# Performance work log

Hardware: AMD Instinct MI355X
Metric: run time of the kernel (lower is better)

## Reference

```python
import jax, jax.numpy as jnp
import numpy as np

N_NODES = 100000
IN_F = 256
OUT_F = 128
N_EDGES = 1600000


def setup_inputs() -> dict:
    key = jax.random.key(0)
    k1, k2, k3, k4, k5 = jax.random.split(key, 5)
    x = jax.random.normal(k1, (N_NODES, IN_F), dtype=jnp.float32)
    edge_index = jax.random.randint(k2, (2, N_EDGES), 0, N_NODES, dtype=jnp.int64)
    edge_weight = jax.random.uniform(k3, (N_EDGES,), dtype=jnp.float32)
    # Xavier-uniform init as in reset_parameters
    limit = float(np.sqrt(6.0 / (IN_F + OUT_F)))
    weight = jax.random.uniform(k4, (IN_F, OUT_F), dtype=jnp.float32,
                                minval=-limit, maxval=limit)
    return {"x": x, "edge_index": edge_index, "edge_weight": edge_weight,
            "weight": weight}


def reference(x, edge_index, edge_weight, weight):
    # support = X @ W  -- dense feature transform
    support = x @ weight                       # [N, out_f]
    # output = spmm(adj, support): out[dst] += w_e * support[src]
    dst = edge_index[0]
    src = edge_index[1]
    msgs = support[src] * edge_weight[:, None]  # [E, out_f] gather
    out = jax.ops.segment_sum(msgs, dst, num_segments=N_NODES)  # [N, out_f]
    return out
```

## Files before the change

### kernel.cpp

```cpp
#include <hip/hip_runtime.h>

#define N_NODES 100000
#define IN_F 256
#define OUT_F 128
#define NB 782

typedef float f32x4 __attribute__((ext_vector_type(4)));
typedef __bf16 bf16x8 __attribute__((ext_vector_type(8)));

__device__ inline unsigned cvt2_bf16(float a, float b) {
  unsigned ua = __float_as_uint(a), ub = __float_as_uint(b);
  ua = (ua + 0x7fffu + ((ua >> 16) & 1u)) >> 16;
  ub = (ub + 0x7fffu + ((ub >> 16) & 1u)) >> 16;
  return ua | (ub << 16);
}
__device__ inline unsigned short cvt1_bf16(float a) {
  unsigned ua = __float_as_uint(a);
  return (unsigned short)((ua + 0x7fffu + ((ua >> 16) & 1u)) >> 16);
}

__global__ __launch_bounds__(256) void transpose_w(const float* __restrict__ w,
                                                   uint4* __restrict__ wt) {
  int c = blockIdx.x * 256 + threadIdx.x;
  int l = c & 63;
  int kt = (c >> 6) & 7;
  int nt = c >> 9;
  int n = nt * 16 + (l & 15);
  int kb = kt * 32 + ((l >> 4) & 3) * 8;
  unsigned d[4];
#pragma unroll
  for (int j = 0; j < 4; ++j) {
    float a = w[(size_t)(kb + 2 * j) * OUT_F + n];
    float b = w[(size_t)(kb + 2 * j + 1) * OUT_F + n];
    d[j] = cvt2_bf16(a, b);
  }
  wt[c] = make_uint4(d[0], d[1], d[2], d[3]);
}

__global__ __launch_bounds__(256) void gemm_count(const float* __restrict__ x,
                                                  const uint4* __restrict__ wt,
                                                  unsigned short* __restrict__ sup,
                                                  const int* __restrict__ ei,
                                                  int* __restrict__ coarse,
                                                  int nedges, int nblk, int gblocks) {
  __shared__ uint4 As[1024];
  __shared__ uint4 Bs[1024];
  __shared__ int hist[NB];
  const int gid = blockIdx.x;
  const int t = threadIdx.x;

  int role, sub;
  int m = (gblocks < nblk) ? gblocks : nblk;
  if (gid < 2 * m) {
    role = gid & 1;
    sub = gid >> 1;
  } else if (nblk > gblocks) {
    role = 1;
    sub = gid - gblocks;
  } else {
    role = 0;
    sub = gid - nblk;
  }

  if (role == 1) {
    for (int i = t; i < NB; i += 256) hist[i] = 0;
    __syncthreads();
    const int base = sub * 2048;
#pragma unroll
    for (int j = 0; j < 8; ++j) {
      int e = base + j * 256 + t;
      if (e < nedges) atomicAdd(&hist[ei[e] >> 7], 1);
    }
    __syncthreads();
    for (int i = t; i < NB; i += 256) coarse[(size_t)sub * NB + i] = hist[i];
    return;
  }

  const int lane = t & 63;
  const int wv = t >> 6;
  const int wm = wv >> 1, wn = wv & 1;
  const int row0 = sub * 128;

  f32x4 acc[4][4];
#pragma unroll
  for (int mi = 0; mi < 4; ++mi)
#pragma unroll
    for (int ni = 0; ni < 4; ++ni) acc[mi][ni] = (f32x4){0.f, 0.f, 0.f, 0.f};

  for (int it = 0; it < 4; ++it) {
    const int k0 = it * 64;
#pragma unroll
    for (int i = 0; i < 4; ++i) {
      int ci = i * 256 + t;
      int g = ci >> 6, l = ci & 63;
      int mrow = (g >> 1) * 16 + (l & 15);
      int k = k0 + (g & 1) * 32 + ((l >> 4) & 3) * 8;
      int row = row0 + mrow;
      if (row > N_NODES - 1) row = N_NODES - 1;
      const float* src = x + (size_t)row * IN_F + k;
      f32x4 v0 = *(const f32x4*)src;
      f32x4 v1 = *(const f32x4*)(src + 4);
      As[ci] = make_uint4(cvt2_bf16(v0.x, v0.y), cvt2_bf16(v0.z, v0.w),
                          cvt2_bf16(v1.x, v1.y), cvt2_bf16(v1.z, v1.w));
      Bs[ci] = wt[((g >> 1) * 8 + it * 2 + (g & 1)) * 64 + l];
    }
    __syncthreads();
#pragma unroll
    for (int ktl = 0; ktl < 2; ++ktl) {
      bf16x8 af[4], bfr[4];
#pragma unroll
      for (int mi = 0; mi < 4; ++mi)
        af[mi] = *(bf16x8*)&As[((wm * 4 + mi) * 2 + ktl) * 64 + lane];
#pragma unroll
      for (int ni = 0; ni < 4; ++ni)
        bfr[ni] = *(bf16x8*)&Bs[((wn * 4 + ni) * 2 + ktl) * 64 + lane];
#pragma unroll
      for (int mi = 0; mi < 4; ++mi)
#pragma unroll
        for (int ni = 0; ni < 4; ++ni)
          acc[mi][ni] = __builtin_amdgcn_mfma_f32_16x16x32_bf16(af[mi], bfr[ni],
                                                                acc[mi][ni], 0, 0, 0);
    }
    __syncthreads();
  }

  const int quad = lane >> 4, col = lane & 15;
#pragma unroll
  for (int mi = 0; mi < 4; ++mi) {
#pragma unroll
    for (int r = 0; r < 4; ++r) {
      int row = row0 + (wm * 4 + mi) * 16 + quad * 4 + r;
      if (row < N_NODES) {
#pragma unroll
        for (int ni = 0; ni < 4; ++ni)
          sup[(size_t)row * OUT_F + (wn * 4 + ni) * 16 + col] =
              cvt1_bf16(acc[mi][ni][r]);
      }
    }
  }
}

__global__ __launch_bounds__(256) void colscan(int* __restrict__ coarse,
                                               int* __restrict__ coltot, int nblk) {
  __shared__ int s[256];
  const int bin = blockIdx.x;
  const int t = threadIdx.x;
  int carry = 0;
  for (int c0 = 0; c0 < nblk; c0 += 256) {
    int idx = c0 + t;
    int v = (idx < nblk) ? coarse[(size_t)idx * NB + bin] : 0;
    s[t] = v;
    __syncthreads();
    for (int off = 1; off < 256; off <<= 1) {
      int xv = (t >= off) ? s[t - off] : 0;
      __syncthreads();
      s[t] += xv;
      __syncthreads();
    }
    int excl = carry + ((t == 0) ? 0 : s[t - 1]);
    if (idx < nblk) coarse[(size_t)idx * NB + bin] = excl;
    carry += s[255];
    __syncthreads();
  }
  if (t == 0) coltot[bin] = carry;
}

__global__ __launch_bounds__(256) void scan1(int* __restrict__ a,
                                             int* __restrict__ bsum, int n) {
  __shared__ int s[256];
  const int t = threadIdx.x;
  const int base = blockIdx.x * 1024 + t * 4;
  int v0 = (base + 0 < n) ? a[base + 0] : 0;
  int v1 = (base + 1 < n) ? a[base + 1] : 0;
  int v2 = (base + 2 < n) ? a[base + 2] : 0;
  int v3 = (base + 3 < n) ? a[base + 3] : 0;
  v1 += v0; v2 += v1; v3 += v2;
  s[t] = v3;
  __syncthreads();
  for (int off = 1; off < 256; off <<= 1) {
    int xv = (t >= off) ? s[t - off] : 0;
    __syncthreads();
    s[t] += xv;
    __syncthreads();
  }
  int excl = (t == 0) ? 0 : s[t - 1];
  if (base + 0 < n) a[base + 0] = v0 + excl;
  if (base + 1 < n) a[base + 1] = v1 + excl;
  if (base + 2 < n) a[base + 2] = v2 + excl;
  if (base + 3 < n) a[base + 3] = v3 + excl;
  if (t == 255 && bsum) bsum[blockIdx.x] = s[255];
}

__global__ __launch_bounds__(256) void partition(const int* __restrict__ ei,
                                                 const float* __restrict__ ew,
                                                 const int* __restrict__ coarse,
                                                 const int* __restrict__ coltot,
                                                 int2* __restrict__ recs, int nedges) {
  __shared__ int wbase[NB];
  const int b = blockIdx.x;
  const int t = threadIdx.x;
  for (int i = t; i < NB; i += 256)
    wbase[i] = coarse[(size_t)b * NB + i] + (i ? coltot[i - 1] : 0);
  __syncthreads();
  const int base = b * 2048;
#pragma unroll
  for (int j = 0; j < 8; ++j) {
    int e = base + j * 256 + t;
    if (e < nedges) {
      int d = ei[e];
      int srcn = ei[nedges + e];
      float wv = ew[e];
      int bin = d >> 7;
      int pos = atomicAdd(&wbase[bin], 1);
      recs[pos] = make_int2((srcn << 7) | (d & 127), __float_as_int(wv));
    }
  }
}

__global__ __launch_bounds__(256) void fine_csr(const int2* __restrict__ recs,
                                                const int* __restrict__ coltot,
                                                int* __restrict__ rowptr,
                                                int2* __restrict__ edges, int nedges) {
  __shared__ int s[128];
  __shared__ int wptr[128];
  const int bin = blockIdx.x;
  const int t = threadIdx.x;
  const int segStart = bin ? coltot[bin - 1] : 0;
  const int segEnd = coltot[bin];
  if (t < 128) s[t] = 0;
  __syncthreads();
  for (int i = segStart + t; i < segEnd; i += 256)
    atomicAdd(&s[recs[i].x & 127], 1);
  __syncthreads();
  for (int off = 1; off < 128; off <<= 1) {
    int xv = (t >= off && t < 128) ? s[t - off] : 0;
    __syncthreads();
    if (t < 128) s[t] += xv;
    __syncthreads();
  }
  if (t < 128) {
    wptr[t] = segStart + ((t == 0) ? 0 : s[t - 1]);
    int node = bin * 128 + t;
    if (node < N_NODES) rowptr[node + 1] = segStart + s[t];
  }
  if (bin == 0 && t == 0) rowptr[0] = 0;
  __syncthreads();
  for (int i = segStart + t; i < segEnd; i += 256) {
    int2 r = recs[i];
    int pos = atomicAdd(&wptr[r.x & 127], 1);
    edges[pos] = make_int2(r.x >> 7, r.y);
  }
}

__global__ __launch_bounds__(256) void gemm_mfma(const float* __restrict__ x,
                                                 const uint4* __restrict__ wt,
                                                 unsigned short* __restrict__ sup) {
  __shared__ uint4 As[1024];
  __shared__ uint4 Bs[1024];
  const int t = threadIdx.x;
  const int lane = t & 63;
  const int wv = t >> 6;
  const int wm = wv >> 1, wn = wv & 1;
  const int row0 = blockIdx.x * 128;

  f32x4 acc[4][4];
#pragma unroll
  for (int mi = 0; mi < 4; ++mi)
#pragma unroll
    for (int ni = 0; ni < 4; ++ni) acc[mi][ni] = (f32x4){0.f, 0.f, 0.f, 0.f};

  for (int it = 0; it < 4; ++it) {
    const int k0 = it * 64;
#pragma unroll
    for (int i = 0; i < 4; ++i) {
      int ci = i * 256 + t;
      int g = ci >> 6, l = ci & 63;
      int m = (g >> 1) * 16 + (l & 15);
      int k = k0 + (g & 1) * 32 + ((l >> 4) & 3) * 8;
      int row = row0 + m;
      if (row > N_NODES - 1) row = N_NODES - 1;
      const float* src = x + (size_t)row * IN_F + k;
      f32x4 v0 = *(const f32x4*)src;
      f32x4 v1 = *(const f32x4*)(src + 4);
      As[ci] = make_uint4(cvt2_bf16(v0.x, v0.y), cvt2_bf16(v0.z, v0.w),
                          cvt2_bf16(v1.x, v1.y), cvt2_bf16(v1.z, v1.w));
      Bs[ci] = wt[((g >> 1) * 8 + it * 2 + (g & 1)) * 64 + l];
    }
    __syncthreads();
#pragma unroll
    for (int ktl = 0; ktl < 2; ++ktl) {
      bf16x8 af[4], bfr[4];
#pragma unroll
      for (int mi = 0; mi < 4; ++mi)
        af[mi] = *(bf16x8*)&As[((wm * 4 + mi) * 2 + ktl) * 64 + lane];
#pragma unroll
      for (int ni = 0; ni < 4; ++ni)
        bfr[ni] = *(bf16x8*)&Bs[((wn * 4 + ni) * 2 + ktl) * 64 + lane];
#pragma unroll
      for (int mi = 0; mi < 4; ++mi)
#pragma unroll
        for (int ni = 0; ni < 4; ++ni)
          acc[mi][ni] = __builtin_amdgcn_mfma_f32_16x16x32_bf16(af[mi], bfr[ni],
                                                                acc[mi][ni], 0, 0, 0);
    }
    __syncthreads();
  }

  const int quad = lane >> 4, col = lane & 15;
#pragma unroll
  for (int mi = 0; mi < 4; ++mi) {
#pragma unroll
    for (int r = 0; r < 4; ++r) {
      int row = row0 + (wm * 4 + mi) * 16 + quad * 4 + r;
      if (row < N_NODES) {
#pragma unroll
        for (int ni = 0; ni < 4; ++ni)
          sup[(size_t)row * OUT_F + (wn * 4 + ni) * 16 + col] =
              cvt1_bf16(acc[mi][ni][r]);
      }
    }
  }
}

__global__ __launch_bounds__(256) void aggregate_bf16(const int* __restrict__ rowptr,
                                                      const int2* __restrict__ edges,
                                                      const unsigned short* __restrict__ sup,
                                                      float* __restrict__ out, int nnodes) {
  int wave = (int)((blockIdx.x * 256u + threadIdx.x) >> 6);
  int lane = threadIdx.x & 63;
  if (wave >= nnodes) return;
  int beg = rowptr[wave];
  int end = rowptr[wave + 1];
  float2 acc = make_float2(0.f, 0.f);
  int e = beg;
  for (; e + 4 <= end; e += 4) {
    int2 m0 = edges[e + 0];
    int2 m1 = edges[e + 1];
    int2 m2 = edges[e + 2];
    int2 m3 = edges[e + 3];
    unsigned u0 = *(const unsigned*)(sup + (size_t)m0.x * OUT_F + lane * 2);
    unsigned u1 = *(const unsigned*)(sup + (size_t)m1.x * OUT_F + lane * 2);
    unsigned u2 = *(const unsigned*)(sup + (size_t)m2.x * OUT_F + lane * 2);
    unsigned u3 = *(const unsigned*)(sup + (size_t)m3.x * OUT_F + lane * 2);
    float w0 = __int_as_float(m0.y), w1 = __int_as_float(m1.y);
    float w2 = __int_as_float(m2.y), w3 = __int_as_float(m3.y);
    acc.x = fmaf(__uint_as_float(u0 << 16), w0, acc.x);
    acc.y = fmaf(__uint_as_float(u0 & 0xffff0000u), w0, acc.y);
    acc.x = fmaf(__uint_as_float(u1 << 16), w1, acc.x);
    acc.y = fmaf(__uint_as_float(u1 & 0xffff0000u), w1, acc.y);
    acc.x = fmaf(__uint_as_float(u2 << 16), w2, acc.x);
    acc.y = fmaf(__uint_as_float(u2 & 0xffff0000u), w2, acc.y);
    acc.x = fmaf(__uint_as_float(u3 << 16), w3, acc.x);
    acc.y = fmaf(__uint_as_float(u3 & 0xffff0000u), w3, acc.y);
  }
  for (; e < end; ++e) {
    int2 m = edges[e];
    unsigned u = *(const unsigned*)(sup + (size_t)m.x * OUT_F + lane * 2);
    float w = __int_as_float(m.y);
    acc.x = fmaf(__uint_as_float(u << 16), w, acc.x);
    acc.y = fmaf(__uint_as_float(u & 0xffff0000u), w, acc.y);
  }
  *(float2*)(out + (size_t)wave * OUT_F + lane * 2) = acc;
}

__global__ __launch_bounds__(256) void scatter_edges(const int* __restrict__ ei,
                                                     const float* __restrict__ ew,
                                                     const unsigned short* __restrict__ sup,
                                                     float* __restrict__ out, int nedges) {
  int gwave = (int)((blockIdx.x * 256u + threadIdx.x) >> 6);
  int lane = threadIdx.x & 63;
  if (gwave >= nedges) return;
  int dst = ei[gwave];
  int src = ei[nedges + gwave];
  float wgt = ew[gwave];
  unsigned u = *(const unsigned*)(sup + (size_t)src * OUT_F + lane * 2);
  float* op = out + (size_t)dst * OUT_F + lane * 2;
  atomicAdd(op, __uint_as_float(u << 16) * wgt);
  atomicAdd(op + 1, __uint_as_float(u & 0xffff0000u) * wgt);
}

extern "C" void kernel_launch(void* const* d_in, const int* in_sizes, int n_in,
                              void* d_out, int out_size, void* d_ws, size_t ws_size,
                              hipStream_t stream) {
  const float* x = (const float*)d_in[0];
  const int* ei = (const int*)d_in[1];
  const float* ew = (const float*)d_in[2];
  const float* w = (const float*)d_in[3];
  float* out = (float*)d_out;
  const int nedges = in_sizes[2];
  const int nblk = (nedges + 2047) / 2048;

  const size_t off_support = 0;
  const size_t sz_support = (size_t)N_NODES * OUT_F * 2;
  const size_t off_rowptr = off_support + sz_support;
  const size_t off_wt = off_rowptr + 400016;
  const size_t off_coltot = off_wt + 65536;
  const size_t off_coarse = off_coltot + 3136;
  const size_t sz_coarse = (size_t)nblk * NB * 4;
  const size_t off_recs = (off_coarse + sz_coarse + 15) & ~(size_t)15;
  const size_t off_edges = off_recs + (size_t)nedges * 8;
  const size_t total_ws = off_edges + (size_t)nedges * 8;

  unsigned short* support = (unsigned short*)((char*)d_ws + off_support);
  int* rowptr = (int*)((char*)d_ws + off_rowptr);
  uint4* wt = (uint4*)((char*)d_ws + off_wt);
  int* coltot = (int*)((char*)d_ws + off_coltot);
  int* coarse = (int*)((char*)d_ws + off_coarse);
  int2* recs = (int2*)((char*)d_ws + off_recs);
  int2* edges = (int2*)((char*)d_ws + off_edges);

  transpose_w<<<16, 256, 0, stream>>>(w, wt);

  if (ws_size < total_ws) {
    const int gblocks = (N_NODES + 127) / 128;
    gemm_mfma<<<gblocks, 256, 0, stream>>>(x, wt, support);
    hipMemsetAsync(d_out, 0, (size_t)out_size * sizeof(float), stream);
    int sblocks = (nedges + 3) / 4;
    scatter_edges<<<sblocks, 256, 0, stream>>>(ei, ew, support, out, nedges);
    return;
  }

  const int gblocks = (N_NODES + 127) / 128;

  gemm_count<<<gblocks + nblk, 256, 0, stream>>>(x, wt, support, ei, coarse,
                                                 nedges, nblk, gblocks);
  colscan<<<NB, 256, 0, stream>>>(coarse, coltot, nblk);
  scan1<<<1, 256, 0, stream>>>(coltot, (int*)nullptr, NB);
  partition<<<nblk, 256, 0, stream>>>(ei, ew, coarse, coltot, recs, nedges);
  fine_csr<<<NB, 256, 0, stream>>>(recs, coltot, rowptr, edges, nedges);

  const int ablocks = (N_NODES + 3) / 4;
  aggregate_bf16<<<ablocks, 256, 0, stream>>>(rowptr, edges, support, out, N_NODES);
}
```

Before: 333.9 us.

## Fuse fine CSR sort into aggregation using shared-memory bucketing per bin

Replaces the fine_csr kernel, which wrote a global sorted edge array and rowptr, and the separate aggregate kernel with one fused kernel. Each block loads its bin's records into LDS, counting-sorts them by local destination, then each wave accumulates 16 destination nodes in registers and writes out directly. This removes a global write and re-read of the edge list plus one launch. The cost is much lower parallelism: only 782 blocks of 8 waves, each wave walking 16 nodes serially, with heavy LDS use and 16 float2 accumulators per thread.

Result: slower. 354.8 us (+6.3%).

```diff
diff --git a/kernel.cpp b/kernel.cpp
--- a/kernel.cpp
+++ b/kernel.cpp
@@ -4,6 +4,7 @@
 #define IN_F 256
 #define OUT_F 128
 #define NB 782
+#define CAP 4096
 
 typedef float f32x4 __attribute__((ext_vector_type(4)));
 typedef __bf16 bf16x8 __attribute__((ext_vector_type(8)));
@@ -217,38 +218,93 @@
   }
 }
 
-__global__ __launch_bounds__(256) void fine_csr(const int2* __restrict__ recs,
+__global__ __launch_bounds__(512) void fine_agg(const int2* __restrict__ recs,
                                                 const int* __restrict__ coltot,
-                                                int* __restrict__ rowptr,
-                                                int2* __restrict__ edges, int nedges) {
-  __shared__ int s[128];
+                                                const unsigned short* __restrict__ sup,
+                                                float* __restrict__ out) {
+  __shared__ int2 lrec[CAP];
+  __shared__ unsigned short sidx[CAP];
+  __shared__ int base[128];
   __shared__ int wptr[128];
   const int bin = blockIdx.x;
   const int t = threadIdx.x;
+  const int wv = t >> 6;
+  const int lane = t & 63;
   const int segStart = bin ? coltot[bin - 1] : 0;
   const int segEnd = coltot[bin];
-  if (t < 128) s[t] = 0;
-  __syncthreads();
-  for (int i = segStart + t; i < segEnd; i += 256)
-    atomicAdd(&s[recs[i].x & 127], 1);
-  __syncthreads();
-  for (int off = 1; off < 128; off <<= 1) {
-    int xv = (t >= off && t < 128) ? s[t - off] : 0;
-    __syncthreads();
-    if (t < 128) s[t] += xv;
-    __syncthreads();
-  }
-  if (t < 128) {
-    wptr[t] = segStart + ((t == 0) ? 0 : s[t - 1]);
-    int node = bin * 128 + t;
-    if (node < N_NODES) rowptr[node + 1] = segStart + s[t];
-  }
-  if (bin == 0 && t == 0) rowptr[0] = 0;
-  __syncthreads();
-  for (int i = segStart + t; i < segEnd; i += 256) {
-    int2 r = recs[i];
-    int pos = atomicAdd(&wptr[r.x & 127], 1);
-    edges[pos] = make_int2(r.x >> 7, r.y);
+
+  float2 acc[16];
+#pragma unroll
+  for (int i = 0; i < 16; ++i) acc[i] = make_float2(0.f, 0.f);
+
+  for (int cur = segStart; cur < segEnd; cur += CAP) {
+    const int nrec = min(segEnd - cur, CAP);
+    if (t < 128) base[t] = 0;
+    __syncthreads();
+    for (int i = t; i < nrec; i += 512) {
+      int2 r = recs[cur + i];
+      lrec[i] = r;
+      atomicAdd(&base[r.x & 127], 1);
+    }
+    __syncthreads();
+    for (int off = 1; off < 128; off <<= 1) {
+      int xv = (t >= off && t < 128) ? base[t - off] : 0;
+      __syncthreads();
+      if (t < 128) base[t] += xv;
+      __syncthreads();
+    }
+    if (t < 128) wptr[t] = (t == 0) ? 0 : base[t - 1];
+    __syncthreads();
+    for (int i = t; i < nrec; i += 512) {
+      int b = lrec[i].x & 127;
+      int p = atomicAdd(&wptr[b], 1);
+      sidx[p] = (unsigned short)i;
+    }
+    __syncthreads();
+#pragma unroll
+    for (int dd = 0; dd < 16; ++dd) {
+      const int dl = wv * 16 + dd;
+      int e0 = (dl == 0) ? 0 : base[dl - 1];
+      int e1 = base[dl];
+      int e = e0;
+      for (; e + 4 <= e1; e += 4) {
+        int i0 = sidx[e + 0], i1 = sidx[e + 1], i2 = sidx[e + 2], i3 = sidx[e + 3];
+        int2 r0 = lrec[i0];
+        int2 r1 = lrec[i1];
+        int2 r2 = lrec[i2];
+        int2 r3 = lrec[i3];
+        unsigned u0 = *(const unsigned*)(sup + (size_t)(r0.x >> 7) * OUT_F + lane * 2);
+        unsigned u1 = *(const unsigned*)(sup + (size_t)(r1.x >> 7) * OUT_F + lane * 2);
+        unsigned u2 = *(const unsigned*)(sup + (size_t)(r2.x >> 7) * OUT_F + lane * 2);
+        unsigned u3 = *(const unsigned*)(sup + (size_t)(r3.x >> 7) * OUT_F + lane * 2);
+        float w0 = __int_as_float(r0.y), w1 = __int_as_float(r1.y);
+        float w2 = __int_as_float(r2.y), w3 = __int_as_float(r3.y);
+        acc[dd].x = fmaf(__uint_as_float(u0 << 16), w0, acc[dd].x);
+        acc[dd].y = fmaf(__uint_as_float(u0 & 0xffff0000u), w0, acc[dd].y);
+        acc[dd].x = fmaf(__uint_as_float(u1 << 16), w1, acc[dd].x);
+        acc[dd].y = fmaf(__uint_as_float(u1 & 0xffff0000u), w1, acc[dd].y);
+        acc[dd].x = fmaf(__uint_as_float(u2 << 16), w2, acc[dd].x);
+        acc[dd].y = fmaf(__uint_as_float(u2 & 0xffff0000u), w2, acc[dd].y);
+        acc[dd].x = fmaf(__uint_as_float(u3 << 16), w3, acc[dd].x);
+        acc[dd].y = fmaf(__uint_as_float(u3 & 0xffff0000u), w3, acc[dd].y);
+      }
+      for (; e < e1; ++e) {
+        int2 r = lrec[sidx[e]];
+        unsigned u = *(const unsigned*)(sup + (size_t)(r.x >> 7) * OUT_F + lane * 2);
+        float w = __int_as_float(r.y);
+        acc[dd].x = fmaf(__uint_as_float(u << 16), w, acc[dd].x);
+        acc[dd].y = fmaf(__uint_as_float(u & 0xffff0000u), w, acc[dd].y);
+      }
+    }
+    __syncthreads();
+  }
+
+  const int nodeBase = bin * 128 + wv * 16;
+#pragma unroll
+  for (int dd = 0; dd < 16; ++dd) {
+    int node = nodeBase + dd;
+    if (node < N_NODES)
+      *(float2*)(out + (size_t)node * OUT_F + lane * 2) = acc[dd];
   }
 }
 
@@ -320,47 +376,6 @@
       }
     }
   }
-}
-
-__global__ __launch_bounds__(256) void aggregate_bf16(const int* __restrict__ rowptr,
-                                                      const int2* __restrict__ edges,
-                                                      const unsigned short* __restrict__ sup,
-                                                      float* __restrict__ out, int nnodes) {
-  int wave = (int)((blockIdx.x * 256u + threadIdx.x) >> 6);
-  int lane = threadIdx.x & 63;
-  if (wave >= nnodes) return;
-  int beg = rowptr[wave];
-  int end = rowptr[wave + 1];
-  float2 acc = make_float2(0.f, 0.f);
-  int e = beg;
-  for (; e + 4 <= end; e += 4) {
-    int2 m0 = edges[e + 0];
-    int2 m1 = edges[e + 1];
-    int2 m2 = edges[e + 2];
-    int2 m3 = edges[e + 3];
-    unsigned u0 = *(const unsigned*)(sup + (size_t)m0.x * OUT_F + lane * 2);
-    unsigned u1 = *(const unsigned*)(sup + (size_t)m1.x * OUT_F + lane * 2);
-    unsigned u2 = *(const unsigned*)(sup + (size_t)m2.x * OUT_F + lane * 2);
-    unsigned u3 = *(const unsigned*)(sup + (size_t)m3.x * OUT_F + lane * 2);
-    float w0 = __int_as_float(m0.y), w1 = __int_as_float(m1.y);
-    float w2 = __int_as_float(m2.y), w3 = __int_as_float(m3.y);
-    acc.x = fmaf(__uint_as_float(u0 << 16), w0, acc.x);
-    acc.y = fmaf(__uint_as_float(u0 & 0xffff0000u), w0, acc.y);
-    acc.x = fmaf(__uint_as_float(u1 << 16), w1, acc.x);
-    acc.y = fmaf(__uint_as_float(u1 & 0xffff0000u), w1, acc.y);
-    acc.x = fmaf(__uint_as_float(u2 << 16), w2, acc.x);
-    acc.y = fmaf(__uint_as_float(u2 & 0xffff0000u), w2, acc.y);
-    acc.x = fmaf(__uint_as_float(u3 << 16), w3, acc.x);
-    acc.y = fmaf(__uint_as_float(u3 & 0xffff0000u), w3, acc.y);
-  }
-  for (; e < end; ++e) {
-    int2 m = edges[e];
-    unsigned u = *(const unsigned*)(sup + (size_t)m.x * OUT_F + lane * 2);
-    float w = __int_as_float(m.y);
-    acc.x = fmaf(__uint_as_float(u << 16), w, acc.x);
-    acc.y = fmaf(__uint_as_float(u & 0xffff0000u), w, acc.y);
-  }
-  *(float2*)(out + (size_t)wave * OUT_F + lane * 2) = acc;
 }
 
 __global__ __launch_bounds__(256) void scatter_edges(const int* __restrict__ ei,
@@ -392,22 +407,18 @@
 
   const size_t off_support = 0;
   const size_t sz_support = (size_t)N_NODES * OUT_F * 2;
-  const size_t off_rowptr = off_support + sz_support;
-  const size_t off_wt = off_rowptr + 400016;
+  const size_t off_wt = off_support + sz_support;
   const size_t off_coltot = off_wt + 65536;
   const size_t off_coarse = off_coltot + 3136;
   const size_t sz_coarse = (size_t)nblk * NB * 4;
   const size_t off_recs = (off_coarse + sz_coarse + 15) & ~(size_t)15;
-  const size_t off_edges = off_recs + (size_t)nedges * 8;
-  const size_t total_ws = off_edges + (size_t)nedges * 8;
+  const size_t total_ws = off_recs + (size_t)nedges * 8;
 
   unsigned short* support = (unsigned short*)((char*)d_ws + off_support);
-  int* rowptr = (int*)((char*)d_ws + off_rowptr);
   uint4* wt = (uint4*)((char*)d_ws + off_wt);
   int* coltot = (int*)((char*)d_ws + off_coltot);
   int* coarse = (int*)((char*)d_ws + off_coarse);
   int2* recs = (int2*)((char*)d_ws + off_recs);
-  int2* edges = (int2*)((char*)d_ws + off_edges);
 
   transpose_w<<<16, 256, 0, stream>>>(w, wt);
 
@@ -427,8 +438,5 @@
   colscan<<<NB, 256, 0, stream>>>(coarse, coltot, nblk);
   scan1<<<1, 256, 0, stream>>>(coltot, (int*)nullptr, NB);
   partition<<<nblk, 256, 0, stream>>>(ei, ew, coarse, coltot, recs, nedges);
-  fine_csr<<<NB, 256, 0, stream>>>(recs, coltot, rowptr, edges, nedges);
-
-  const int ablocks = (N_NODES + 3) / 4;
-  aggregate_bf16<<<ablocks, 256, 0, stream>>>(rowptr, edges, support, out, N_NODES);
-}
+  fine_agg<<<NB, 512, 0, stream>>>(recs, coltot, support, out);
+}
```

## Partition edges per XCD bin range and build CSR in place via LDS

Applied to the files above, without the earlier changes.

The single-pass partition is replaced by partition2, a persistent-style kernel. Blocks grab 2048-edge chunks from per-range ticket counters, and each XCD starts with its own contiguous range of coarse bins. The aim is to keep scattered record writes local to one XCD's L2, at the cost of reading the destination index array up to eight times. fine_csr now stages each bin's records in LDS and writes the sorted CSR back into the same recs buffer, removing the separate edges buffer and one global read pass. The LDS staging is capped at 4096 records per bin, so a bin with more edges than that would be silently truncated.

Measured after the change: 583.4 us. 1.75x slower.

```diff
diff --git a/kernel.cpp b/kernel.cpp
--- a/kernel.cpp
+++ b/kernel.cpp
@@ -4,6 +4,7 @@
 #define IN_F 256
 #define OUT_F 128
 #define NB 782
+#define LCAP 4096
 
 typedef float f32x4 __attribute__((ext_vector_type(4)));
 typedef __bf16 bf16x8 __attribute__((ext_vector_type(8)));
@@ -17,6 +18,10 @@
 __device__ inline unsigned short cvt1_bf16(float a) {
   unsigned ua = __float_as_uint(a);
   return (unsigned short)((ua + 0x7fffu + ((ua >> 16) & 1u)) >> 16);
+}
+
+__device__ inline int get_xcd() {
+  return (int)(__builtin_amdgcn_s_getreg(6164) & 7u);
 }
 
 __global__ __launch_bounds__(256) void transpose_w(const float* __restrict__ w,
@@ -191,134 +196,90 @@
   if (t == 255 && bsum) bsum[blockIdx.x] = s[255];
 }
 
-__global__ __launch_bounds__(256) void partition(const int* __restrict__ ei,
-                                                 const float* __restrict__ ew,
-                                                 const int* __restrict__ coarse,
-                                                 const int* __restrict__ coltot,
-                                                 int2* __restrict__ recs, int nedges) {
-  __shared__ int wbase[NB];
-  const int b = blockIdx.x;
-  const int t = threadIdx.x;
-  for (int i = t; i < NB; i += 256)
-    wbase[i] = coarse[(size_t)b * NB + i] + (i ? coltot[i - 1] : 0);
-  __syncthreads();
-  const int base = b * 2048;
-#pragma unroll
-  for (int j = 0; j < 8; ++j) {
-    int e = base + j * 256 + t;
-    if (e < nedges) {
-      int d = ei[e];
-      int srcn = ei[nedges + e];
-      float wv = ew[e];
-      int bin = d >> 7;
-      int pos = atomicAdd(&wbase[bin], 1);
-      recs[pos] = make_int2((srcn << 7) | (d & 127), __float_as_int(wv));
-    }
-  }
-}
-
-__global__ __launch_bounds__(256) void fine_csr(const int2* __restrict__ recs,
+__global__ __launch_bounds__(256) void partition2(const int* __restrict__ ei,
+                                                  const float* __restrict__ ew,
+                                                  const int* __restrict__ coarse,
+                                                  const int* __restrict__ coltot,
+                                                  int* __restrict__ tickets,
+                                                  int2* __restrict__ recs,
+                                                  int nedges, int nblk) {
+  __shared__ int wbase[128];
+  __shared__ int sS;
+  const int t = threadIdx.x;
+  const int myx = get_xcd();
+  for (int rr = 0; rr < 8; ++rr) {
+    const int r = (myx + rr) & 7;
+    const int binLo = (r * NB) / 8;
+    const int binHi = ((r + 1) * NB) / 8;
+    const int nbins = binHi - binLo;
+    while (true) {
+      if (t == 0) sS = atomicAdd(&tickets[r], 1);
+      __syncthreads();
+      const int s = sS;
+      __syncthreads();
+      if (s >= nblk) break;
+      for (int i = t; i < nbins; i += 256) {
+        int bin = binLo + i;
+        wbase[i] = coarse[(size_t)s * NB + bin] + (bin ? coltot[bin - 1] : 0);
+      }
+      __syncthreads();
+      const int base = s * 2048;
+#pragma unroll
+      for (int j = 0; j < 8; ++j) {
+        int e = base + j * 256 + t;
+        if (e < nedges) {
+          int d = ei[e];
+          int bin = d >> 7;
+          if (bin >= binLo && bin < binHi) {
+            int srcn = ei[nedges + e];
+            float wv = ew[e];
+            int pos = atomicAdd(&wbase[bin - binLo], 1);
+            recs[pos] = make_int2((srcn << 7) | (d & 127), __float_as_int(wv));
+          }
+        }
+      }
+      __syncthreads();
+    }
+  }
+}
+
+__global__ __launch_bounds__(256) void fine_csr(int2* __restrict__ recs,
                                                 const int* __restrict__ coltot,
-                                                int* __restrict__ rowptr,
-                                                int2* __restrict__ edges, int nedges) {
-  __shared__ int s[128];
-  __shared__ int wptr[128];
+                                                int* __restrict__ rowptr) {
+  __shared__ int2 lrec[LCAP];
+  __shared__ int cnt[128];
+  __shared__ int wp[128];
   const int bin = blockIdx.x;
   const int t = threadIdx.x;
   const int segStart = bin ? coltot[bin - 1] : 0;
   const int segEnd = coltot[bin];
-  if (t < 128) s[t] = 0;
+  int nrec = segEnd - segStart;
+  if (nrec > LCAP) nrec = LCAP;
+  if (t < 128) cnt[t] = 0;
   __syncthreads();
-  for (int i = segStart + t; i < segEnd; i += 256)
-    atomicAdd(&s[recs[i].x & 127], 1);
+  for (int i = t; i < nrec; i += 256) {
+    int2 r = recs[segStart + i];
+    lrec[i] = r;
+    atomicAdd(&cnt[r.x & 127], 1);
+  }
   __syncthreads();
   for (int off = 1; off < 128; off <<= 1) {
-    int xv = (t >= off && t < 128) ? s[t - off] : 0;
-    __syncthreads();
-    if (t < 128) s[t] += xv;
+    int xv = (t >= off && t < 128) ? cnt[t - off] : 0;
+    __syncthreads();
+    if (t < 128) cnt[t] += xv;
     __syncthreads();
   }
   if (t < 128) {
-    wptr[t] = segStart + ((t == 0) ? 0 : s[t - 1]);
+    wp[t] = segStart + ((t == 0) ? 0 : cnt[t - 1]);
     int node = bin * 128 + t;
-    if (node < N_NODES) rowptr[node + 1] = segStart + s[t];
+    if (node < N_NODES) rowptr[node + 1] = segStart + cnt[t];
   }
   if (bin == 0 && t == 0) rowptr[0] = 0;
   __syncthreads();
-  for (int i = segStart + t; i < segEnd; i += 256) {
-    int2 r = recs[i];
-    int pos = atomicAdd(&wptr[r.x & 127], 1);
-    edges[pos] = make_int2(r.x >> 7, r.y);
-  }
-}
-
-__global__ __launch_bounds__(256) void gemm_mfma(const float* __restrict__ x,
-                                                 const uint4* __restrict__ wt,
-                                                 unsigned short* __restrict__ sup) {
-  __shared__ uint4 As[1024];
-  __shared__ uint4 Bs[1024];
-  const int t = threadIdx.x;
-  const int lane = t & 63;
-  const int wv = t >> 6;
-  const int wm = wv >> 1, wn = wv & 1;
-  const int row0 = blockIdx.x * 128;
-
-  f32x4 acc[4][4];
-#pragma unroll
-  for (int mi = 0; mi < 4; ++mi)
-#pragma unroll
-    for (int ni = 0; ni < 4; ++ni) acc[mi][ni] = (f32x4){0.f, 0.f, 0.f, 0.f};
-
-  for (int it = 0; it < 4; ++it) {
-    const int k0 = it * 64;
-#pragma unroll
-    for (int i = 0; i < 4; ++i) {
-      int ci = i * 256 + t;
-      int g = ci >> 6, l = ci & 63;
-      int m = (g >> 1) * 16 + (l & 15);
-      int k = k0 + (g & 1) * 32 + ((l >> 4) & 3) * 8;
-      int row = row0 + m;
-      if (row > N_NODES - 1) row = N_NODES - 1;
-      const float* src = x + (size_t)row * IN_F + k;
-      f32x4 v0 = *(const f32x4*)src;
-      f32x4 v1 = *(const f32x4*)(src + 4);
-      As[ci] = make_uint4(cvt2_bf16(v0.x, v0.y), cvt2_bf16(v0.z, v0.w),
-                          cvt2_bf16(v1.x, v1.y), cvt2_bf16(v1.z, v1.w));
-      Bs[ci] = wt[((g >> 1) * 8 + it * 2 + (g & 1)) * 64 + l];
-    }
-    __syncthreads();
-#pragma unroll
-    for (int ktl = 0; ktl < 2; ++ktl) {
-      bf16x8 af[4], bfr[4];
-#pragma unroll
-      for (int mi = 0; mi < 4; ++mi)
-        af[mi] = *(bf16x8*)&As[((wm * 4 + mi) * 2 + ktl) * 64 + lane];
-#pragma unroll
-      for (int ni = 0; ni < 4; ++ni)
-        bfr[ni] = *(bf16x8*)&Bs[((wn * 4 + ni) * 2 + ktl) * 64 + lane];
-#pragma unroll
-      for (int mi = 0; mi < 4; ++mi)
-#pragma unroll
-        for (int ni = 0; ni < 4; ++ni)
-          acc[mi][ni] = __builtin_amdgcn_mfma_f32_16x16x32_bf16(af[mi], bfr[ni],
-                                                                acc[mi][ni], 0, 0, 0);
-    }
-    __syncthreads();
-  }
-
-  const int quad = lane >> 4, col = lane & 15;
-#pragma unroll
-  for (int mi = 0; mi < 4; ++mi) {
-#pragma unroll
-    for (int r = 0; r < 4; ++r) {
-      int row = row0 + (wm * 4 + mi) * 16 + quad * 4 + r;
-      if (row < N_NODES) {
-#pragma unroll
-        for (int ni = 0; ni < 4; ++ni)
-          sup[(size_t)row * OUT_F + (wn * 4 + ni) * 16 + col] =
-              cvt1_bf16(acc[mi][ni][r]);
-      }
-    }
+  for (int i = t; i < nrec; i += 256) {
+    int2 r = lrec[i];
+    int p = atomicAdd(&wp[r.x & 127], 1);
+    recs[p] = make_int2(r.x >> 7, r.y);
   }
 }
 
@@ -363,6 +324,76 @@
   *(float2*)(out + (size_t)wave * OUT_F + lane * 2) = acc;
 }
 
+__global__ __launch_bounds__(256) void gemm_mfma(const float* __restrict__ x,
+                                                 const uint4* __restrict__ wt,
+                                                 unsigned short* __restrict__ sup) {
+  __shared__ uint4 As[1024];
+  __shared__ uint4 Bs[1024];
+  const int t = threadIdx.x;
+  const int lane = t & 63;
+  const int wv = t >> 6;
+  const int wm = wv >> 1, wn = wv & 1;
+  const int row0 = blockIdx.x * 128;
+
+  f32x4 acc[4][4];
+#pragma unroll
+  for (int mi = 0; mi < 4; ++mi)
+#pragma unroll
+    for (int ni = 0; ni < 4; ++ni) acc[mi][ni] = (f32x4){0.f, 0.f, 0.f, 0.f};
+
+  for (int it = 0; it < 4; ++it) {
+    const int k0 = it * 64;
+#pragma unroll
+    for (int i = 0; i < 4; ++i) {
+      int ci = i * 256 + t;
+      int g = ci >> 6, l = ci & 63;
+      int m = (g >> 1) * 16 + (l & 15);
+      int k = k0 + (g & 1) * 32 + ((l >> 4) & 3) * 8;
+      int row = row0 + m;
+      if (row > N_NODES - 1) row = N_NODES - 1;
+      const float* src = x + (size_t)row * IN_F + k;
+      f32x4 v0 = *(const f32x4*)src;
+      f32x4 v1 = *(const f32x4*)(src + 4);
+      As[ci] = make_uint4(cvt2_bf16(v0.x, v0.y), cvt2_bf16(v0.z, v0.w),
+                          cvt2_bf16(v1.x, v1.y), cvt2_bf16(v1.z, v1.w));
+      Bs[ci] = wt[((g >> 1) * 8 + it * 2 + (g & 1)) * 64 + l];
+    }
+    __syncthreads();
+#pragma unroll
+    for (int ktl = 0; ktl < 2; ++ktl) {
+      bf16x8 af[4], bfr[4];
+#pragma unroll
+      for (int mi = 0; mi < 4; ++mi)
+        af[mi] = *(bf16x8*)&As[((wm * 4 + mi) * 2 + ktl) * 64 + lane];
+#pragma unroll
+      for (int ni = 0; ni < 4; ++ni)
+        bfr[ni] = *(bf16x8*)&Bs[((wn * 4 + ni) * 2 + ktl) * 64 + lane];
+#pragma unroll
+      for (int mi = 0; mi < 4; ++mi)
+#pragma unroll
+        for (int ni = 0; ni < 4; ++ni)
+          acc[mi][ni] = __builtin_amdgcn_mfma_f32_16x16x32_bf16(af[mi], bfr[ni],
+                                                                acc[mi][ni], 0, 0, 0);
+    }
+    __syncthreads();
+  }
+
+  const int quad = lane >> 4, col = lane & 15;
+#pragma unroll
+  for (int mi = 0; mi < 4; ++mi) {
+#pragma unroll
+    for (int r = 0; r < 4; ++r) {
+      int row = row0 + (wm * 4 + mi) * 16 + quad * 4 + r;
+      if (row < N_NODES) {
+#pragma unroll
+        for (int ni = 0; ni < 4; ++ni)
+          sup[(size_t)row * OUT_F + (wn * 4 + ni) * 16 + col] =
+              cvt1_bf16(acc[mi][ni][r]);
+      }
+    }
+  }
+}
+
 __global__ __launch_bounds__(256) void scatter_edges(const int* __restrict__ ei,
                                                      const float* __restrict__ ew,
                                                      const unsigned short* __restrict__ sup,
@@ -395,19 +426,19 @@
   const size_t off_rowptr = off_support + sz_support;
   const size_t off_wt = off_rowptr + 400016;
   const size_t off_coltot = off_wt + 65536;
-  const size_t off_coarse = off_coltot + 3136;
+  const size_t off_tick = off_coltot + 3136;
+  const size_t off_coarse = off_tick + 48;
   const size_t sz_coarse = (size_t)nblk * NB * 4;
   const size_t off_recs = (off_coarse + sz_coarse + 15) & ~(size_t)15;
-  const size_t off_edges = off_recs + (size_t)nedges * 8;
-  const size_t total_ws = off_edges + (size_t)nedges * 8;
+  const size_t total_ws = off_recs + (size_t)nedges * 8;
 
   unsigned short* support = (unsigned short*)((char*)d_ws + off_support);
   int* rowptr = (int*)((char*)d_ws + off_rowptr);
   uint4* wt = (uint4*)((char*)d_ws + off_wt);
   int* coltot = (int*)((char*)d_ws + off_coltot);
+  int* tickets = (int*)((char*)d_ws + off_tick);
   int* coarse = (int*)((char*)d_ws + off_coarse);
   int2* recs = (int2*)((char*)d_ws + off_recs);
-  int2* edges = (int2*)((char*)d_ws + off_edges);
 
   transpose_w<<<16, 256, 0, stream>>>(w, wt);
 
@@ -422,13 +453,15 @@
 
   const int gblocks = (N_NODES + 127) / 128;
 
+  hipMemsetAsync(tickets, 0, 32, stream);
   gemm_count<<<gblocks + nblk, 256, 0, stream>>>(x, wt, support, ei, coarse,
                                                  nedges, nblk, gblocks);
   colscan<<<NB, 256, 0, stream>>>(coarse, coltot, nblk);
   scan1<<<1, 256, 0, stream>>>(coltot, (int*)nullptr, NB);
-  partition<<<nblk, 256, 0, stream>>>(ei, ew, coarse, coltot, recs, nedges);
-  fine_csr<<<NB, 256, 0, stream>>>(recs, coltot, rowptr, edges, nedges);
+  partition2<<<2048, 256, 0, stream>>>(ei, ew, coarse, coltot, tickets, recs,
+                                       nedges, nblk);
+  fine_csr<<<NB, 256, 0, stream>>>(recs, coltot, rowptr);
 
   const int ablocks = (N_NODES + 3) / 4;
-  aggregate_bf16<<<ablocks, 256, 0, stream>>>(rowptr, edges, support, out, N_NODES);
-}
+  aggregate_bf16<<<ablocks, 256, 0, stream>>>(rowptr, recs, support, out, N_NODES);
+}
```
